# Kernel optimization log

Measured on AMD Instinct MI355X. Metric: run time of the kernel, lower is better.

## Reference

```python
import jax, jax.numpy as jnp
import numpy as np

B, L = 2048, 200
D_MODEL, HIDDEN, V = 512, 256, 40000
LN_EPS = 1e-5


def setup_inputs() -> dict:
    key = jax.random.key(0)
    ks = jax.random.split(key, 10)
    return {
        "hidden": jax.random.normal(ks[0], (B, D_MODEL), dtype=jnp.float32),
        "loc_seq": jax.random.randint(ks[1], (B, L), 0, V, dtype=jnp.int32),
        "mask": jax.random.randint(ks[2], (B, L), 0, 2, dtype=jnp.int32),
        # learned_head params
        "W1": jax.random.normal(ks[3], (D_MODEL, HIDDEN), dtype=jnp.float32) / np.sqrt(D_MODEL),
        "b1": jnp.zeros((HIDDEN,), dtype=jnp.float32),
        "gamma": jnp.ones((HIDDEN,), dtype=jnp.float32),
        "beta": jnp.zeros((HIDDEN,), dtype=jnp.float32),
        "W2": jax.random.normal(ks[4], (HIDDEN, V), dtype=jnp.float32) / np.sqrt(HIDDEN),
        "b2": jnp.zeros((V,), dtype=jnp.float32),
        # scalar weights (match torch init values)
        "recency_weight": jnp.asarray(3.0, dtype=jnp.float32),
        "frequency_weight": jnp.asarray(2.0, dtype=jnp.float32),
        "history_scale": jnp.asarray(8.0, dtype=jnp.float32),
        "learned_scale": jnp.asarray(0.5, dtype=jnp.float32),
    }


def _history_scores(loc_seq, mask, recency_weight, frequency_weight, history_scale):
    # Per-(b,t) contribution: recency term exp(-0.1*(L-1-t))*recency_weight
    # plus frequency term frequency_weight per valid occurrence.
    Lcur = loc_seq.shape[1]
    t = jnp.arange(Lcur, dtype=jnp.float32)
    recency = jnp.exp(-0.1 * (Lcur - 1.0 - t)) * recency_weight  # (L,)
    maskf = mask.astype(jnp.float32)                              # (B,L)
    vals = (recency[None, :] + frequency_weight) * maskf          # (B,L)
    Bcur = loc_seq.shape[0]
    b_idx = jnp.arange(Bcur)[:, None]                             # (B,1)
    scores = jnp.zeros((Bcur, V), dtype=jnp.float32).at[b_idx, loc_seq].add(vals)
    return scores * history_scale


def reference(hidden, loc_seq, mask, W1, b1, gamma, beta, W2, b2,
              recency_weight, frequency_weight, history_scale, learned_scale):
    # learned head: Linear -> LayerNorm -> GELU -> (Dropout inactive in eval) -> Linear
    h = hidden @ W1 + b1                                          # (B,HIDDEN)
    mu = jnp.mean(h, axis=-1, keepdims=True)
    var = jnp.mean(jnp.square(h - mu), axis=-1, keepdims=True)
    h = (h - mu) * jax.lax.rsqrt(var + LN_EPS) * gamma + beta
    h = jax.nn.gelu(h, approximate=False)
    learned_logits = h @ W2 + b2                                  # (B,V)
    hist = _history_scores(loc_seq, mask, recency_weight, frequency_weight, history_scale)
    return learned_logits * learned_scale + hist
```

## Files before the change

### kernel.cpp

```cpp
#include <hip/hip_runtime.h>
#include <hip/hip_bf16.h>

#define B_   2048
#define L_   200
#define DM_  512
#define HID_ 256
#define V_   40000
#define NPAD 40064
#define LN_EPS 1e-5f

typedef short bf16x8 __attribute__((ext_vector_type(8)));
typedef float f32x4  __attribute__((ext_vector_type(4)));

#define GLOAD_LDS16(g, l)                                                     \
    __builtin_amdgcn_global_load_lds(                                         \
        (const __attribute__((address_space(1))) void*)(g),                   \
        (__attribute__((address_space(3))) void*)(l), 16, 0, 0)

__global__ __launch_bounds__(256) void transpose_w2(const float* __restrict__ W2,
                                                    __hip_bfloat16* __restrict__ WT) {
    __shared__ float tile[64][65];
    const int n0 = blockIdx.x * 64;
    const int k0 = blockIdx.y * 64;
    const int tid = threadIdx.x;

    const int c = tid & 63, r4 = tid >> 6;
#pragma unroll
    for (int p = 0; p < 16; ++p) {
        int r = p * 4 + r4;
        int n = n0 + c;
        tile[r][c] = (n < V_) ? W2[(size_t)(k0 + r) * V_ + n] : 0.f;
    }
    __syncthreads();

    const int nl = tid >> 3;
    const int kb = (tid & 7) * 8;
#pragma unroll
    for (int p = 0; p < 2; ++p) {
        int n = p * 32 + nl;
        bf16x8 v;
#pragma unroll
        for (int j = 0; j < 8; ++j) {
            __hip_bfloat16 h = __float2bfloat16(tile[kb + j][n]);
            v[j] = *(short*)&h;
        }
        *(bf16x8*)(WT + (size_t)(n0 + n) * HID_ + k0 + kb) = v;
    }
}

__global__ __launch_bounds__(512) void head_kernel(const float* __restrict__ hidden,
                                                   const float* __restrict__ W1,
                                                   const float* __restrict__ b1,
                                                   const float* __restrict__ gamma,
                                                   const float* __restrict__ beta,
                                                   __hip_bfloat16* __restrict__ hout) {
    __shared__ float hid[8][DM_];
    __shared__ float part[8][HID_];
    __shared__ float red[2][8][4];
    const int r0 = blockIdx.x * 8;
    const int tid = threadIdx.x;
    const int col = tid & 255, half = tid >> 8;

    {
        const float4* src = (const float4*)(hidden + (size_t)r0 * DM_);
        float4* dst = (float4*)(&hid[0][0]);
        for (int i = tid; i < 8 * DM_ / 4; i += 512) dst[i] = src[i];
    }
    __syncthreads();

    float acc[8] = {0.f, 0.f, 0.f, 0.f, 0.f, 0.f, 0.f, 0.f};
    const int kbeg = half * (DM_ / 2);
#pragma unroll 8
    for (int k = kbeg; k < kbeg + DM_ / 2; ++k) {
        float w = W1[(size_t)k * HID_ + col];
#pragma unroll
        for (int r = 0; r < 8; ++r) acc[r] = fmaf(hid[r][k], w, acc[r]);
    }

    if (half == 1) {
#pragma unroll
        for (int r = 0; r < 8; ++r) part[r][col] = acc[r];
    }
    __syncthreads();
    if (half == 0) {
        const float b1v = b1[col], gv = gamma[col], bev = beta[col];
        const int lane = col & 63, wv = col >> 6;
        float v[8];
#pragma unroll
        for (int r = 0; r < 8; ++r) {
            v[r] = acc[r] + part[r][col] + b1v;
            float s = v[r], q = v[r] * v[r];
#pragma unroll
            for (int off = 1; off < 64; off <<= 1) {
                s += __shfl_xor(s, off);
                q += __shfl_xor(q, off);
            }
            if (lane == 0) { red[0][r][wv] = s; red[1][r][wv] = q; }
        }
        __syncthreads();
#pragma unroll
        for (int r = 0; r < 8; ++r) {
            float s  = red[0][r][0] + red[0][r][1] + red[0][r][2] + red[0][r][3];
            float q  = red[1][r][0] + red[1][r][1] + red[1][r][2] + red[1][r][3];
            float mu = s * (1.f / HID_);
            float var = q * (1.f / HID_) - mu * mu;
            float hn = (v[r] - mu) * rsqrtf(var + LN_EPS) * gv + bev;
            float g  = 0.5f * hn * (1.f + erff(hn * 0.70710678118654752f));
            hout[(size_t)(r0 + r) * HID_ + col] = __float2bfloat16(g);
        }
    }
}

#define BM 128
#define BN 128
#define NCT (NPAD / BN)

__global__ __launch_bounds__(256, 1) void gemm_kernel(const __hip_bfloat16* __restrict__ hA,
                                                      const __hip_bfloat16* __restrict__ BT,
                                                      const float* __restrict__ b2,
                                                      const float* __restrict__ lsp,
                                                      float* __restrict__ out) {
    __shared__ __hip_bfloat16 As[BM * HID_];
    __shared__ __hip_bfloat16 Bs[BN * HID_];

    const int g = blockIdx.x;
    const int rt = g / NCT;
    const int ct = g - rt * NCT;
    const int r0 = rt * BM, c0 = ct * BN;

    const int tid = threadIdx.x;
    const int lane = tid & 63;
    const int wv = tid >> 6;
    const int wr = (wv >> 1) * 64;
    const int wc = (wv & 1) * 64;
    const float ls = lsp[0];

    {
        const __hip_bfloat16* aB = hA + (size_t)r0 * HID_;
        const __hip_bfloat16* bB = BT + (size_t)c0 * HID_;
        const int cc = lane & 31;
        const int rhalf = lane >> 5;
#pragma unroll
        for (int i = 0; i < 16; ++i) {
            const int ch = wv * 16 + i;
            const int r = ch * 2 + rhalf;
            const int csrc = cc ^ (r & 7);
            GLOAD_LDS16(aB + (size_t)r * HID_ + csrc * 8, (char*)As + ch * 1024);
            GLOAD_LDS16(bB + (size_t)r * HID_ + csrc * 8, (char*)Bs + ch * 1024);
        }
    }
    __syncthreads();

    f32x4 acc[4][4];
#pragma unroll
    for (int m = 0; m < 4; ++m)
#pragma unroll
        for (int n = 0; n < 4; ++n) acc[m][n] = (f32x4){0.f, 0.f, 0.f, 0.f};

    const int rb = wr + (lane & 15);
    const int cb = wc + (lane & 15);
#pragma unroll
    for (int ks = 0; ks < HID_ / 32; ++ks) {
        const int kb = ks * 32 + ((lane >> 4) << 3);
        const int ke = kb ^ ((lane & 7) << 3);
        bf16x8 af[4], bf[4];
#pragma unroll
        for (int m = 0; m < 4; ++m)
            af[m] = *(const bf16x8*)(As + (size_t)(rb + m * 16) * HID_ + ke);
#pragma unroll
        for (int n = 0; n < 4; ++n)
            bf[n] = *(const bf16x8*)(Bs + (size_t)(cb + n * 16) * HID_ + ke);
#pragma unroll
        for (int m = 0; m < 4; ++m)
#pragma unroll
            for (int n = 0; n < 4; ++n)
                acc[m][n] = __builtin_amdgcn_mfma_f32_16x16x32_bf16(
                    bf[n], af[m], acc[m][n], 0, 0, 0);
    }

    const int orow = r0 + wr + (lane & 15);
    const int ocol = c0 + wc + ((lane >> 4) << 2);
    f32x4 b2v[4];
#pragma unroll
    for (int n = 0; n < 4; ++n) {
        int col = ocol + n * 16;
        b2v[n] = (col < V_) ? *(const f32x4*)(b2 + col)
                            : (f32x4){0.f, 0.f, 0.f, 0.f};
    }
#pragma unroll
    for (int m = 0; m < 4; ++m) {
        float* orp = out + (size_t)(orow + m * 16) * V_;
#pragma unroll
        for (int n = 0; n < 4; ++n) {
            int col = ocol + n * 16;
            if (col < V_) {
                f32x4 o = (acc[m][n] + b2v[n]) * ls;
                __builtin_nontemporal_store(o, (f32x4*)(orp + col));
            }
        }
    }
}

__global__ __launch_bounds__(256) void hist_kernel(const int* __restrict__ loc,
                                                   const int* __restrict__ mask,
                                                   const float* __restrict__ rw,
                                                   const float* __restrict__ fw,
                                                   const float* __restrict__ hs,
                                                   float* __restrict__ out) {
    const int idx = blockIdx.x * 256 + threadIdx.x;
    if (idx >= B_ * L_) return;
    const int b = idx / L_, t = idx - b * L_;
    if (mask[idx] != 0) {
        float recency = expf(-0.1f * (float)(L_ - 1 - t)) * rw[0];
        float val = (recency + fw[0]) * hs[0];
        atomicAdd(out + (size_t)b * V_ + loc[idx], val);
    }
}

extern "C" void kernel_launch(void* const* d_in, const int* in_sizes, int n_in,
                              void* d_out, int out_size, void* d_ws, size_t ws_size,
                              hipStream_t stream) {
    const float* hidden = (const float*)d_in[0];
    const int*   loc    = (const int*)d_in[1];
    const int*   mask   = (const int*)d_in[2];
    const float* W1     = (const float*)d_in[3];
    const float* b1     = (const float*)d_in[4];
    const float* gamma  = (const float*)d_in[5];
    const float* beta   = (const float*)d_in[6];
    const float* W2     = (const float*)d_in[7];
    const float* b2     = (const float*)d_in[8];
    const float* rw     = (const float*)d_in[9];
    const float* fw     = (const float*)d_in[10];
    const float* hs     = (const float*)d_in[11];
    const float* ls     = (const float*)d_in[12];
    float* out = (float*)d_out;

    __hip_bfloat16* WT   = (__hip_bfloat16*)d_ws;
    __hip_bfloat16* hbuf = (__hip_bfloat16*)((char*)d_ws + 20512768);

    transpose_w2<<<dim3(NPAD / 64, HID_ / 64), 256, 0, stream>>>(W2, WT);
    head_kernel<<<B_ / 8, 512, 0, stream>>>(hidden, W1, b1, gamma, beta, hbuf);
    gemm_kernel<<<(B_ / BM) * NCT, 256, 0, stream>>>(hbuf, WT, b2, ls, out);
    hist_kernel<<<(B_ * L_ + 255) / 256, 256, 0, stream>>>(loc, mask, rw, fw, hs, out);
}
```

Before: 217.5 us.

## Restructure GEMM as persistent register-resident A tiles streaming B columns

Replaces the 128x128 LDS-tiled GEMM grid with 256 persistent blocks. Each block keeps a 32-row slice of the hidden activations in registers and walks a quarter of the vocab columns, with each wave taking a contiguous range of 16-column tiles. B fragments are loaded straight from global memory with a two-deep register double buffer, so there is no LDS and no barrier. The aim is to remove LDS staging and barrier costs and to overlap loads with MFMA in an output-store-bound kernel. In exchange, B data is reread from global/L2 by every row block, each MFMA does little work, stores are no longer nontemporal, and register pressure is high.

```diff
diff --git a/kernel.cpp b/kernel.cpp
--- a/kernel.cpp
+++ b/kernel.cpp
@@ -11,11 +11,6 @@
 
 typedef short bf16x8 __attribute__((ext_vector_type(8)));
 typedef float f32x4  __attribute__((ext_vector_type(4)));
-
-#define GLOAD_LDS16(g, l)                                                     \
-    __builtin_amdgcn_global_load_lds(                                         \
-        (const __attribute__((address_space(1))) void*)(g),                   \
-        (__attribute__((address_space(3))) void*)(l), 16, 0, 0)
 
 __global__ __launch_bounds__(256) void transpose_w2(const float* __restrict__ W2,
                                                     __hip_bfloat16* __restrict__ WT) {
@@ -111,94 +106,80 @@
     }
 }
 
-#define BM 128
-#define BN 128
-#define NCT (NPAD / BN)
-
 __global__ __launch_bounds__(256, 1) void gemm_kernel(const __hip_bfloat16* __restrict__ hA,
                                                       const __hip_bfloat16* __restrict__ BT,
                                                       const float* __restrict__ b2,
                                                       const float* __restrict__ lsp,
                                                       float* __restrict__ out) {
-    __shared__ __hip_bfloat16 As[BM * HID_];
-    __shared__ __hip_bfloat16 Bs[BN * HID_];
-
-    const int g = blockIdx.x;
-    const int rt = g / NCT;
-    const int ct = g - rt * NCT;
-    const int r0 = rt * BM, c0 = ct * BN;
-
-    const int tid = threadIdx.x;
-    const int lane = tid & 63;
-    const int wv = tid >> 6;
-    const int wr = (wv >> 1) * 64;
-    const int wc = (wv & 1) * 64;
+    const int b = blockIdx.x;
+    const int x = b & 7;
+    const int i = b >> 3;
+    const int cq = x >> 1;
+    const int rt = ((x & 1) << 5) + i;
+    const int r0 = rt * 32;
+
+    const int lane = threadIdx.x & 63;
+    const int wv = threadIdx.x >> 6;
     const float ls = lsp[0];
 
-    {
-        const __hip_bfloat16* aB = hA + (size_t)r0 * HID_;
-        const __hip_bfloat16* bB = BT + (size_t)c0 * HID_;
-        const int cc = lane & 31;
-        const int rhalf = lane >> 5;
-#pragma unroll
-        for (int i = 0; i < 16; ++i) {
-            const int ch = wv * 16 + i;
-            const int r = ch * 2 + rhalf;
-            const int csrc = cc ^ (r & 7);
-            GLOAD_LDS16(aB + (size_t)r * HID_ + csrc * 8, (char*)As + ch * 1024);
-            GLOAD_LDS16(bB + (size_t)r * HID_ + csrc * 8, (char*)Bs + ch * 1024);
-        }
-    }
-    __syncthreads();
-
-    f32x4 acc[4][4];
-#pragma unroll
-    for (int m = 0; m < 4; ++m)
-#pragma unroll
-        for (int n = 0; n < 4; ++n) acc[m][n] = (f32x4){0.f, 0.f, 0.f, 0.f};
-
-    const int rb = wr + (lane & 15);
-    const int cb = wc + (lane & 15);
-#pragma unroll
-    for (int ks = 0; ks < HID_ / 32; ++ks) {
-        const int kb = ks * 32 + ((lane >> 4) << 3);
-        const int ke = kb ^ ((lane & 7) << 3);
-        bf16x8 af[4], bf[4];
-#pragma unroll
-        for (int m = 0; m < 4; ++m)
-            af[m] = *(const bf16x8*)(As + (size_t)(rb + m * 16) * HID_ + ke);
-#pragma unroll
-        for (int n = 0; n < 4; ++n)
-            bf[n] = *(const bf16x8*)(Bs + (size_t)(cb + n * 16) * HID_ + ke);
-#pragma unroll
-        for (int m = 0; m < 4; ++m)
-#pragma unroll
-            for (int n = 0; n < 4; ++n)
-                acc[m][n] = __builtin_amdgcn_mfma_f32_16x16x32_bf16(
-                    bf[n], af[m], acc[m][n], 0, 0, 0);
-    }
-
-    const int orow = r0 + wr + (lane & 15);
-    const int ocol = c0 + wc + ((lane >> 4) << 2);
-    f32x4 b2v[4];
-#pragma unroll
-    for (int n = 0; n < 4; ++n) {
-        int col = ocol + n * 16;
-        b2v[n] = (col < V_) ? *(const f32x4*)(b2 + col)
-                            : (f32x4){0.f, 0.f, 0.f, 0.f};
-    }
-#pragma unroll
-    for (int m = 0; m < 4; ++m) {
-        float* orp = out + (size_t)(orow + m * 16) * V_;
-#pragma unroll
-        for (int n = 0; n < 4; ++n) {
-            int col = ocol + n * 16;
-            if (col < V_) {
-                f32x4 o = (acc[m][n] + b2v[n]) * ls;
-                __builtin_nontemporal_store(o, (f32x4*)(orp + col));
-            }
-        }
-    }
+    const int rlo  = lane & 15;
+    const int koff = (lane >> 4) << 3;
+    const int c4   = (lane >> 4) << 2;
+
+    bf16x8 af[2][8];
+#pragma unroll
+    for (int g = 0; g < 2; ++g)
+#pragma unroll
+        for (int ks = 0; ks < 8; ++ks)
+            af[g][ks] = *(const bf16x8*)(hA + (size_t)(r0 + 16 * g + rlo) * HID_
+                                             + ks * 32 + koff);
+
+    const int qbase = cq * 625;
+    const int cbeg = qbase + ((wv == 0) ? 0 : 157 + (wv - 1) * 156);
+    const int cend = qbase + ((wv == 0) ? 157 : 157 + wv * 156);
+
+    float* outw = out + (size_t)(r0 + rlo) * V_;
+    const size_t rowstep = (size_t)16 * V_;
+
+#define LOADB(bq, bv, c)                                                      \
+    {                                                                         \
+        const int col0 = (c) * 16;                                            \
+        _Pragma("unroll")                                                     \
+        for (int ks = 0; ks < 8; ++ks)                                        \
+            bq[ks] = *(const bf16x8*)(BT + (size_t)(col0 + rlo) * HID_        \
+                                          + ks * 32 + koff);                  \
+        bv = *(const f32x4*)(b2 + col0 + c4);                                 \
+    }
+
+#define COMPUTE_STORE(bq, bv, c)                                              \
+    {                                                                         \
+        f32x4 a0 = (f32x4){0.f, 0.f, 0.f, 0.f};                               \
+        f32x4 a1 = (f32x4){0.f, 0.f, 0.f, 0.f};                               \
+        _Pragma("unroll")                                                     \
+        for (int ks = 0; ks < 8; ++ks) {                                      \
+            a0 = __builtin_amdgcn_mfma_f32_16x16x32_bf16(bq[ks], af[0][ks],   \
+                                                         a0, 0, 0, 0);        \
+            a1 = __builtin_amdgcn_mfma_f32_16x16x32_bf16(bq[ks], af[1][ks],   \
+                                                         a1, 0, 0, 0);        \
+        }                                                                     \
+        const int col = (c) * 16 + c4;                                        \
+        *(f32x4*)(outw + col)           = (a0 + bv) * ls;                     \
+        *(f32x4*)(outw + rowstep + col) = (a1 + bv) * ls;                     \
+    }
+
+    bf16x8 bq0[8], bq1[8];
+    f32x4 bv0, bv1;
+    LOADB(bq0, bv0, cbeg);
+    int c = cbeg;
+    for (; c + 2 <= cend; c += 2) {
+        LOADB(bq1, bv1, c + 1);
+        COMPUTE_STORE(bq0, bv0, c);
+        if (c + 2 < cend) LOADB(bq0, bv0, c + 2);
+        COMPUTE_STORE(bq1, bv1, c + 1);
+    }
+    if (c < cend) COMPUTE_STORE(bq0, bv0, c);
+#undef LOADB
+#undef COMPUTE_STORE
 }
 
 __global__ __launch_bounds__(256) void hist_kernel(const int* __restrict__ loc,
@@ -240,6 +221,6 @@
 
     transpose_w2<<<dim3(NPAD / 64, HID_ / 64), 256, 0, stream>>>(W2, WT);
     head_kernel<<<B_ / 8, 512, 0, stream>>>(hidden, W1, b1, gamma, beta, hbuf);
-    gemm_kernel<<<(B_ / BM) * NCT, 256, 0, stream>>>(hbuf, WT, b2, ls, out);
+    gemm_kernel<<<256, 256, 0, stream>>>(hbuf, WT, b2, ls, out);
     hist_kernel<<<(B_ * L_ + 255) / 256, 256, 0, stream>>>(loc, mask, rw, fw, hs, out);
 }
```

New measurement: 262.6 us. +20.7%, slower.
